# Kernel tuning notes

Hardware: AMD Instinct MI355X
Metric: run time of the kernel (lower is better)

The kernel has to match this reference:

```python
import jax, jax.numpy as jnp
import numpy as np

B, C_IN, C_OUT = 32, 64, 128
K_SIZE, STRIDE, PAD, H = 3, 1, 1, 56
H_OUT = (H + 2 * PAD - K_SIZE) // STRIDE + 1


def setup_inputs() -> dict:
    key = jax.random.key(0)
    kx, kw = jax.random.split(key)
    x = jax.random.normal(kx, (B, C_IN, H, H), dtype=jnp.float32)
    # kaiming_uniform-ish init for K of shape [kh, kw, C_in, C_out]
    fan_in = K_SIZE * C_IN * C_OUT  # torch fan_in for this layout (dim1 * receptive field)
    bound = np.sqrt(6.0 / fan_in).astype(np.float32)
    K = jax.random.uniform(kw, (K_SIZE, K_SIZE, C_IN, C_OUT), dtype=jnp.float32,
                           minval=-bound, maxval=bound)
    return {"x": x, "K": K}


def reference(x, K):
    # Faithful to the torch code INCLUDING its mismatched flatten orders:
    #   patch flattened as (C_in, kh, kw); K flattened as (kh, kw, C_in).
    xp = jnp.pad(x, ((0, 0), (0, 0), (PAD, PAD), (PAD, PAD)))
    end = (H_OUT - 1) * STRIDE + 1
    # patches[b, c, di, dj, i, j] = xp[b, c, i*stride+di, j*stride+dj]
    rows = []
    for di in range(K_SIZE):
        cols = []
        for dj in range(K_SIZE):
            cols.append(xp[:, :, di:di + end:STRIDE, dj:dj + end:STRIDE])  # [B,C,Ho,Wo]
        rows.append(jnp.stack(cols, axis=2))  # [B,C,kw,Ho,Wo]
    patches = jnp.stack(rows, axis=2)  # [B, C, kh, kw, Ho, Wo]
    # flatten patch in (C, kh, kw) order -> [B, Ho, Wo, C*kh*kw]
    p = patches.transpose(0, 4, 5, 1, 2, 3).reshape(B, H_OUT, H_OUT, -1)
    # K flattened in (kh, kw, C) order, exactly as K.view(-1, out_channels)
    Kf = K.reshape(-1, C_OUT)  # [kh*kw*C_in, C_out]
    out = p @ Kf  # [B, Ho, Wo, C_out]
    return out.transpose(0, 3, 1, 2)  # [B, C_out, Ho, Wo]
```

## Files before the change

kernel.cpp:

```cpp
#include <hip/hip_runtime.h>
#include <hip/hip_bf16.h>
#include <stdint.h>


#define B_   32
#define CIN  64
#define COUT 128
#define H_   56
#define HP   58
#define F_   576

typedef __attribute__((ext_vector_type(8))) short bf16x8;
typedef __attribute__((ext_vector_type(4))) float f32x4;

#define XP_ELEMS (B_*HP*HP*CIN)
#define XP_SLACK 4096
#define XP_TOTAL (XP_ELEMS + XP_SLACK)
#define WG_ELEMS (COUT*F_)
#define WS_NEEDED ((size_t)(XP_TOTAL + WG_ELEMS) * 2)

#define NROW   (B_*HP)
#define NWBLK  (WG_ELEMS/256)

__global__ __launch_bounds__(256) void prep_all(const float* __restrict__ x,
                                                const float* __restrict__ K,
                                                __hip_bfloat16* __restrict__ xpT,
                                                __hip_bfloat16* __restrict__ WgT) {
  const int id = blockIdx.x;
  const int t  = threadIdx.x;

  if (id > NROW) {
    int n = (id - (NROW + 1))*256 + t;
    int co = n / F_, g = n % F_;
    int di = g / 192, dj = (g % 192) / 64, c = g & 63;
    int f  = c*9 + di*3 + dj;
    int kh = f / 192, kw = (f % 192) / 64, cc = f & 63;
    WgT[n] = __float2bfloat16(K[(((size_t)kh*3 + kw)*CIN + cc)*COUT + co]);
    return;
  }
  if (id == NROW) {
    bf16x8 z = (bf16x8)0;
    for (int idx = t; idx < XP_SLACK/8; idx += 256)
      ((bf16x8*)(xpT + XP_ELEMS))[idx] = z;
    return;
  }

  const int b = id / HP, h = id % HP;
  __hip_bfloat16* orow = xpT + (size_t)(b*HP + h) * HP * CIN;
  if (h == 0 || h == HP-1) {
    bf16x8 z = (bf16x8)0;
    for (int idx = t; idx < HP*CIN/8; idx += 256) ((bf16x8*)orow)[idx] = z;
    return;
  }
  __shared__ __align__(16) float tile[CIN][60];
  const float* xrow = x + ((size_t)(b*CIN)*H_ + (h-1)) * H_;
  for (int idx = t; idx < CIN*(H_/4); idx += 256) {
    int c = idx / 14, w4 = idx % 14;
    f32x4 v = *(const f32x4*)(xrow + (size_t)c*H_*H_ + w4*4);
    *(f32x4*)&tile[c][w4*4] = v;
  }
  __syncthreads();
  for (int idx = t; idx < HP*8; idx += 256) {
    int w = idx >> 3, cg = (idx & 7) * 8;
    __align__(16) __hip_bfloat16 tmp[8];
    if (w == 0 || w == HP-1) {
#pragma unroll
      for (int k2 = 0; k2 < 8; ++k2) tmp[k2] = __float2bfloat16(0.f);
    } else {
#pragma unroll
      for (int k2 = 0; k2 < 8; ++k2) tmp[k2] = __float2bfloat16(tile[cg + k2][w-1]);
    }
    *(bf16x8*)(orow + (size_t)w*CIN + cg) = *(const bf16x8*)tmp;
  }
}

__global__ __launch_bounds__(256, 2) void conv_mfma(
    const __hip_bfloat16* __restrict__ xpT,
    const __hip_bfloat16* __restrict__ WgT,
    float* __restrict__ out) {
  __shared__ __align__(16) char lds[65536];
  const int t    = threadIdx.x;
  const int wave = t >> 6;
  const int l    = t & 63;
  const int lr   = l & 15, lq = l >> 4;
  const int wr   = wave >> 1, wc = wave & 1;

  const int bid = blockIdx.x;
  const int swz = (bid & 7) * 112 + (bid >> 3);
  const int bb  = swz / 28;
  const int i0  = (swz % 28) * 2;

  f32x4 acc[4][4];
#pragma unroll
  for (int mi = 0; mi < 4; ++mi)
#pragma unroll
    for (int ni = 0; ni < 4; ++ni) acc[mi][ni] = (f32x4)0.f;

  const char* xb    = (const char*)xpT + (size_t)bb*HP*HP*CIN*2;
  const char* wbase = (const char*)WgT;

  auto stage = [&](int q, int buf) {
    const int di = q / 3, dj = q % 3;
    char* Ab = lds + buf*32768;
    char* Bb = Ab + 16384;
#pragma unroll
    for (int s = 0; s < 4; ++s) {
      int o = s*4096 + t*16;
      int m = o >> 7;
      const char* src = xb
          + (size_t)((i0 + (m >> 6) + di)*HP + dj + (m & 63)) * (CIN*2)
          + ((o & 127) ^ ((m & 7) << 4));
      __builtin_amdgcn_global_load_lds(
          (const __attribute__((address_space(1))) void*)src,
          (__attribute__((address_space(3))) void*)(Ab + s*4096 + wave*1024),
          16, 0, 0);
    }
    const char* wg = wbase + q*128;
#pragma unroll
    for (int s = 0; s < 4; ++s) {
      int o  = s*4096 + t*16;
      int co = o >> 7;
      const char* src = wg + (size_t)co*1152 + ((o & 127) ^ ((co & 7) << 4));
      __builtin_amdgcn_global_load_lds(
          (const __attribute__((address_space(1))) void*)src,
          (__attribute__((address_space(3))) void*)(Bb + s*4096 + wave*1024),
          16, 0, 0);
    }
  };

  stage(0, 0);
  __syncthreads();

  for (int q = 0; q < 9; ++q) {
    const int buf = q & 1;
    if (q + 1 < 9) stage(q + 1, buf ^ 1);
    const char* Ab = lds + buf*32768;
    const char* Bb = Ab + 16384;
#pragma unroll
    for (int ks = 0; ks < 2; ++ks) {
      bf16x8 a[4], bfr[4];
      const int cb = ks*64 + lq*16;
#pragma unroll
      for (int mi = 0; mi < 4; ++mi) {
        int m = wr*64 + mi*16 + lr;
        a[mi] = *(const bf16x8*)(Ab + (((m << 7) | cb) ^ ((m & 7) << 4)));
      }
#pragma unroll
      for (int ni = 0; ni < 4; ++ni) {
        int co = wc*64 + ni*16 + lr;
        bfr[ni] = *(const bf16x8*)(Bb + (((co << 7) | cb) ^ ((co & 7) << 4)));
      }
#pragma unroll
      for (int mi = 0; mi < 4; ++mi)
#pragma unroll
        for (int ni = 0; ni < 4; ++ni)
          acc[mi][ni] = __builtin_amdgcn_mfma_f32_16x16x32_bf16(
              a[mi], bfr[ni], acc[mi][ni], 0, 0, 0);
    }
    __syncthreads();
  }

#pragma unroll
  for (int mi = 0; mi < 4; ++mi) {
    int j0 = mi*16 + lq*4;
    if (j0 < H_) {
      int i = i0 + wr;
#pragma unroll
      for (int ni = 0; ni < 4; ++ni) {
        int co = wc*64 + ni*16 + lr;
        float* dst = out + (((size_t)(bb*COUT + co))*H_ + i)*H_ + j0;
        *(f32x4*)dst = acc[mi][ni];
      }
    }
  }
}

__global__ __launch_bounds__(256) void conv_naive(const float* __restrict__ x,
                                                  const float* __restrict__ K,
                                                  float* __restrict__ out) {
  int idx = blockIdx.x*256 + threadIdx.x;
  const int total = B_*COUT*H_*H_;
  if (idx >= total) return;
  int j = idx % H_, i = (idx / H_) % H_, co = (idx / (H_*H_)) % COUT, b = idx / (H_*H_*COUT);
  float s = 0.f;
  for (int c = 0; c < CIN; ++c)
    for (int di = 0; di < 3; ++di) {
      int ii = i + di - 1;
      if (ii < 0 || ii >= H_) continue;
      for (int dj = 0; dj < 3; ++dj) {
        int jj = j + dj - 1;
        if (jj < 0 || jj >= H_) continue;
        int f = c*9 + di*3 + dj;
        int kh = f / 192, kw = (f % 192) / 64, cc = f & 63;
        s += x[(((size_t)b*CIN + c)*H_ + ii)*H_ + jj] *
             K[(((size_t)kh*3 + kw)*CIN + cc)*COUT + co];
      }
    }
  out[idx] = s;
}

extern "C" void kernel_launch(void* const* d_in, const int* in_sizes, int n_in,
                              void* d_out, int out_size, void* d_ws, size_t ws_size,
                              hipStream_t stream) {
  const float* x = (const float*)d_in[0];
  const float* K = (const float*)d_in[1];
  float* out = (float*)d_out;
  if (ws_size >= WS_NEEDED) {
    __hip_bfloat16* xpT = (__hip_bfloat16*)d_ws;
    __hip_bfloat16* WgT = xpT + XP_TOTAL;
    prep_all<<<NROW + 1 + NWBLK, 256, 0, stream>>>(x, K, xpT, WgT);
    conv_mfma<<<B_*28, 256, 0, stream>>>(xpT, WgT, out);
  } else {
    conv_naive<<<(B_*COUT*H_*H_ + 255)/256, 256, 0, stream>>>(x, K, out);
  }
}
```

Measured before the change: 42.86 us.

## Load input halo once per block and compute four output rows per block

Each block now covers four output rows (not two) and all 128 output channels. It loads the whole 6-row padded input halo into LDS once, instead of re-staging shifted A tiles for each of the 9 filter taps. Per-tap A fragments are read from LDS at shifted offsets with an XOR swizzle, and only the weight tiles stay double-buffered. This removes the redundant global loads of the input across taps, but doubles the accumulator registers per wave, halves the grid size, and raises LDS use per block, which may reduce occupancy.

Measured after the change: 40.93 us. 1.05x faster.

```diff
diff --git a/kernel.cpp b/kernel.cpp
--- a/kernel.cpp
+++ b/kernel.cpp
@@ -21,6 +21,10 @@
 
 #define NROW   (B_*HP)
 #define NWBLK  (WG_ELEMS/256)
+
+#define A_STAGE 45056
+#define A_ALLOC 45568
+#define LDS_TOT (A_ALLOC + 2*16384)
 
 __global__ __launch_bounds__(256) void prep_all(const float* __restrict__ x,
                                                 const float* __restrict__ K,
@@ -78,44 +82,40 @@
     const __hip_bfloat16* __restrict__ xpT,
     const __hip_bfloat16* __restrict__ WgT,
     float* __restrict__ out) {
-  __shared__ __align__(16) char lds[65536];
+  __shared__ __align__(16) char lds[LDS_TOT];
   const int t    = threadIdx.x;
   const int wave = t >> 6;
   const int l    = t & 63;
   const int lr   = l & 15, lq = l >> 4;
-  const int wr   = wave >> 1, wc = wave & 1;
 
   const int bid = blockIdx.x;
-  const int swz = (bid & 7) * 112 + (bid >> 3);
-  const int bb  = swz / 28;
-  const int i0  = (swz % 28) * 2;
-
-  f32x4 acc[4][4];
+  const int swz = (bid & 7) * 56 + (bid >> 3);
+  const int bb  = swz / 14;
+  const int i0  = (swz % 14) * 4;
+
+  f32x4 acc[4][8];
 #pragma unroll
   for (int mi = 0; mi < 4; ++mi)
 #pragma unroll
-    for (int ni = 0; ni < 4; ++ni) acc[mi][ni] = (f32x4)0.f;
-
-  const char* xb    = (const char*)xpT + (size_t)bb*HP*HP*CIN*2;
+    for (int ni = 0; ni < 8; ++ni) acc[mi][ni] = (f32x4)0.f;
+
+  const char* xb    = (const char*)xpT + (size_t)(bb*HP + i0) * HP * CIN * 2;
   const char* wbase = (const char*)WgT;
 
-  auto stage = [&](int q, int buf) {
-    const int di = q / 3, dj = q % 3;
-    char* Ab = lds + buf*32768;
-    char* Bb = Ab + 16384;
-#pragma unroll
-    for (int s = 0; s < 4; ++s) {
-      int o = s*4096 + t*16;
-      int m = o >> 7;
-      const char* src = xb
-          + (size_t)((i0 + (m >> 6) + di)*HP + dj + (m & 63)) * (CIN*2)
-          + ((o & 127) ^ ((m & 7) << 4));
-      __builtin_amdgcn_global_load_lds(
-          (const __attribute__((address_space(1))) void*)src,
-          (__attribute__((address_space(3))) void*)(Ab + s*4096 + wave*1024),
-          16, 0, 0);
-    }
+#pragma unroll
+  for (int s = 0; s < 11; ++s) {
+    int o = s*4096 + t*16;
+    int m = o >> 7;
+    const char* src = xb + ((o & ~127) | ((o & 127) ^ ((m & 7) << 4)));
+    __builtin_amdgcn_global_load_lds(
+        (const __attribute__((address_space(1))) void*)src,
+        (__attribute__((address_space(3))) void*)(lds + s*4096 + wave*1024),
+        16, 0, 0);
+  }
+
+  auto stageB = [&](int q, int buf) {
     const char* wg = wbase + q*128;
+    char* Bb = lds + A_ALLOC + buf*16384;
 #pragma unroll
     for (int s = 0; s < 4; ++s) {
       int o  = s*4096 + t*16;
@@ -128,46 +128,51 @@
     }
   };
 
-  stage(0, 0);
+  stageB(0, 0);
   __syncthreads();
 
+#pragma unroll
   for (int q = 0; q < 9; ++q) {
     const int buf = q & 1;
-    if (q + 1 < 9) stage(q + 1, buf ^ 1);
-    const char* Ab = lds + buf*32768;
-    const char* Bb = Ab + 16384;
+    if (q < 8) stageB(q + 1, buf ^ 1);
+    const char* Bb = lds + A_ALLOC + buf*16384;
 #pragma unroll
     for (int ks = 0; ks < 2; ++ks) {
-      bf16x8 a[4], bfr[4];
+      const int kg  = q*64 + ks*32;
+      const int di  = kg / 192;
+      const int rem = kg - di*192;
+      bf16x8 a[4], bfr[8];
+#pragma unroll
+      for (int mi = 0; mi < 4; ++mi) {
+        int r   = (wave + di)*58 + mi*16 + lr;
+        int tot = r*128 + rem*2 + lq*16;
+        int adr = (tot & ~127) | ((tot & 127) ^ (((tot >> 7) & 7) << 4));
+        a[mi] = *(const bf16x8*)(lds + adr);
+      }
       const int cb = ks*64 + lq*16;
 #pragma unroll
-      for (int mi = 0; mi < 4; ++mi) {
-        int m = wr*64 + mi*16 + lr;
-        a[mi] = *(const bf16x8*)(Ab + (((m << 7) | cb) ^ ((m & 7) << 4)));
-      }
-#pragma unroll
-      for (int ni = 0; ni < 4; ++ni) {
-        int co = wc*64 + ni*16 + lr;
+      for (int ni = 0; ni < 8; ++ni) {
+        int co = ni*16 + lr;
         bfr[ni] = *(const bf16x8*)(Bb + (((co << 7) | cb) ^ ((co & 7) << 4)));
       }
 #pragma unroll
       for (int mi = 0; mi < 4; ++mi)
 #pragma unroll
-        for (int ni = 0; ni < 4; ++ni)
+        for (int ni = 0; ni < 8; ++ni)
           acc[mi][ni] = __builtin_amdgcn_mfma_f32_16x16x32_bf16(
               a[mi], bfr[ni], acc[mi][ni], 0, 0, 0);
     }
     __syncthreads();
   }
 
+  const int i = i0 + wave;
 #pragma unroll
   for (int mi = 0; mi < 4; ++mi) {
     int j0 = mi*16 + lq*4;
     if (j0 < H_) {
-      int i = i0 + wr;
-#pragma unroll
-      for (int ni = 0; ni < 4; ++ni) {
-        int co = wc*64 + ni*16 + lr;
+#pragma unroll
+      for (int ni = 0; ni < 8; ++ni) {
+        int co = ni*16 + lr;
         float* dst = out + (((size_t)(bb*COUT + co))*H_ + i)*H_ + j0;
         *(f32x4*)dst = acc[mi][ni];
       }
@@ -209,7 +214,7 @@
     __hip_bfloat16* xpT = (__hip_bfloat16*)d_ws;
     __hip_bfloat16* WgT = xpT + XP_TOTAL;
     prep_all<<<NROW + 1 + NWBLK, 256, 0, stream>>>(x, K, xpT, WgT);
-    conv_mfma<<<B_*28, 256, 0, stream>>>(xpT, WgT, out);
+    conv_mfma<<<B_*14, 256, 0, stream>>>(xpT, WgT, out);
   } else {
     conv_naive<<<(B_*COUT*H_*H_ + 255)/256, 256, 0, stream>>>(x, K, out);
   }
```
